# Kernel tuning notes

Measured on AMD Instinct MI355X. Metric: run time of the kernel, lower is better.

Reference implementation:

```python
import jax, jax.numpy as jnp
import numpy as np

B, N, D = 256, 128, 128            # batch, tree nodes (incl. zero-pad node 0), input_feature_dim
MAX_PRED, MAX_COL, MAX_OP = 30, 200, 20
OTHER = D - 2 * MAX_PRED - 1 - 32  # 35
C_IN = D + 64 - 2 * MAX_PRED - 1   # 131 = tree-conv input channels


def setup_inputs() -> dict:
    key = jax.random.key(0)
    ks = jax.random.split(key, 14)
    others = jax.random.normal(ks[0], (B, N, OTHER), dtype=jnp.float32)
    cols = jax.random.randint(ks[1], (B, N, MAX_PRED), 0, MAX_COL).astype(jnp.float32)
    ops = jax.random.randint(ks[2], (B, N, MAX_PRED), 0, MAX_OP).astype(jnp.float32)
    length = jax.random.randint(ks[3], (B, N, 1), 0, MAX_PRED + 1).astype(jnp.float32)
    param = jax.random.normal(ks[4], (B, N, 32), dtype=jnp.float32)
    feature = jnp.concatenate([others, cols, ops, length, param], axis=-1).transpose(0, 2, 1)  # (B, D, N)
    indexes = jax.random.randint(ks[5], (B, 3 * (N - 1), 1), 0, N, dtype=jnp.int32).astype(jnp.int64)

    def conv_w(k, o, i):
        return jax.random.normal(k, (o, i, 3), dtype=jnp.float32) * (1.0 / np.sqrt(3 * i))

    def lin_w(k, o, i):
        return jax.random.normal(k, (o, i), dtype=jnp.float32) * (1.0 / np.sqrt(i))

    return dict(
        feature=feature, indexes=indexes,
        col_embed=jax.random.normal(ks[6], (MAX_COL, 32), dtype=jnp.float32),
        op_embed=jax.random.normal(ks[7], (MAX_OP, 32), dtype=jnp.float32),
        w1=conv_w(ks[8], 256, C_IN), b1=jnp.zeros((256,), jnp.float32),
        w2=conv_w(ks[9], 128, 256), b2=jnp.zeros((128,), jnp.float32),
        w3=conv_w(ks[10], 64, 128), b3=jnp.zeros((64,), jnp.float32),
        fw1=lin_w(ks[11], 32, 64), fb1=jnp.zeros((32,), jnp.float32),
        fw2=lin_w(ks[12], 1, 32), fb2=jnp.zeros((1,), jnp.float32),
    )


def tree_conv(x, idx, w, b):
    # x: (B, C, N); idx: (B, 3M, 1) with M = N-1; w: (O, C, 3)
    Bb, C, _ = x.shape
    g = jnp.take_along_axis(x, idx[:, :, 0][:, None, :], axis=2)        # (B, C, 3M) gather (self,left,right)
    g = g.reshape(Bb, C, -1, 3)                                          # (B, C, M, 3)
    out = jnp.einsum('bcmk,ock->bom', g, w) + b[None, :, None]           # stride-3 kernel-3 conv
    zero = jnp.zeros((Bb, w.shape[0], 1), out.dtype)                     # re-prepend zero-pad node
    return jnp.concatenate([zero, out], axis=2)                          # (B, O, N)


def tree_norm(x):
    # per-sample layernorm over (channel, node) dims, unbiased std (torch.std default)
    mean = jnp.mean(x, axis=(1, 2), keepdims=True)
    std = jnp.std(x, axis=(1, 2), ddof=1, keepdims=True)
    return (x - mean) / (std + 1e-5)


def reference(feature, indexes, col_embed, op_embed, w1, b1, w2, b2, w3, b3, fw1, fb1, fw2, fb2):
    Bb, d, n = feature.shape
    f = feature.transpose(0, 2, 1).reshape(Bb * n, d)
    others = f[:, :OTHER]
    cols = jax.lax.stop_gradient(f[:, OTHER:OTHER + MAX_PRED]).astype(jnp.int32)
    ops = jax.lax.stop_gradient(f[:, OTHER + MAX_PRED:OTHER + 2 * MAX_PRED]).astype(jnp.int32)
    length = f[:, OTHER + 2 * MAX_PRED:OTHER + 2 * MAX_PRED + 1]          # (BN, 1)
    param = f[:, -32:]
    emb = jnp.concatenate([col_embed[cols], op_embed[ops]], axis=-1)      # (BN, P, 64)
    mask = jnp.arange(MAX_PRED)[None, :] < length                         # (BN, P)
    total = jnp.sum(emb * mask[..., None], axis=1)                        # (BN, 64) masked sum
    collate = jnp.concatenate([others, total, param], axis=-1).reshape(Bb, n, -1).transpose(0, 2, 1)  # (B, C_IN, N)

    x = jax.nn.leaky_relu(tree_norm(tree_conv(collate, indexes, w1, b1)), 0.01)
    x = jax.nn.leaky_relu(tree_norm(tree_conv(x, indexes, w2, b2)), 0.01)
    x = tree_norm(tree_conv(x, indexes, w3, b3))                          # (B, 64, N)
    pooled = jnp.max(x, axis=2)                                           # DynamicPooling -> (B, 64)
    h = jax.nn.relu(pooled @ fw1.T + fb1)
    return h @ fw2.T + fb2                                                # (B, 1)
```

## Files before the change

kernel.cpp:

```cpp
#include <hip/hip_runtime.h>
#include <hip/hip_bf16.h>
#include <math.h>

#define B_    256
#define N_    128
#define MAXP  30
#define OTHER_ 35
#define CIN1  131
#define NIDX  381

#define KPAD1 160
#define KPAD2 256
#define KPAD3 128
#define S_IDX (B_ * NIDX)
#define S_P1  (15 * 2 * 8 * 512)
#define S_P2  (24 * 2 * 4 * 512)
#define S_P3  (12 * 2 * 2 * 512)
#define PREP_TOTAL (S_IDX + S_P1 + S_P2 + S_P3)
#define PREP_BLOCKS ((PREP_TOTAL + 511) / 512)
#define EMBED_BLOCKS (B_ * 4)

typedef short short8 __attribute__((ext_vector_type(8)));
typedef float f32x4 __attribute__((ext_vector_type(4)));

__device__ inline void split1(float v, short& h, short& l) {
  unsigned u = __float_as_uint(v);
  unsigned hb = (u + 0x7fffu + ((u >> 16) & 1u)) >> 16;
  float fh = __uint_as_float(hb << 16);
  float r = v - fh;
  unsigned u2 = __float_as_uint(r);
  unsigned lb = (u2 + 0x7fffu + ((u2 >> 16) & 1u)) >> 16;
  h = (short)hb;
  l = (short)lb;
}

__device__ inline void split2(float v, short& h, short& l) {
  __hip_bfloat16 hb = __float2bfloat16(v);
  float fh = __bfloat162float(hb);
  __hip_bfloat16 lb = __float2bfloat16(v - fh);
  __builtin_memcpy(&h, &hb, 2);
  __builtin_memcpy(&l, &lb, 2);
}

template <int KREAL, int KPAD, int SUB, int NWO>
__device__ inline void packw(int l, const float* __restrict__ w,
                             short* __restrict__ oh, short* __restrict__ ol) {
  const int e = l & 7;
  const int lane = (l >> 3) & 63;
  const int x = l >> 9;
  const int su = x % SUB;
  const int y = x / SUB;
  const int g = y % NWO;
  const int gks = y / NWO;
  const int oc = (g * SUB + su) * 16 + (lane & 15);
  const int ctot = gks * 32 + ((lane >> 4) & 3) * 8 + e;
  const int kk = ctot / KPAD;
  const int ch = ctot - kk * KPAD;
  const float v = (ch < KREAL) ? w[(oc * KREAL + ch) * 3 + kk] : 0.f;
  short h, lo;
  split1(v, h, lo);
  oh[l] = h;
  ol[l] = lo;
}

__global__ __launch_bounds__(512) void prep_embed_kernel(
    const float* __restrict__ feature,
    const float* __restrict__ col_embed,
    const float* __restrict__ op_embed,
    short* __restrict__ collateH, short* __restrict__ collateL,
    const void* __restrict__ rawIdx, int* __restrict__ idx32,
    const float* __restrict__ w1, short* __restrict__ w1h, short* __restrict__ w1l,
    const float* __restrict__ w2, short* __restrict__ w2h, short* __restrict__ w2l,
    const float* __restrict__ w3, short* __restrict__ w3h, short* __restrict__ w3l) {
  const int bx = blockIdx.x;
  const int tid = threadIdx.x;

  if (bx >= EMBED_BLOCKS) {
    const int gid = (bx - EMBED_BLOCKS) * 512 + tid;
    if (gid < S_IDX) {
      const int* r32 = (const int*)rawIdx;
      const int lane = tid & 63;
      const int lo = r32[2 * lane];
      const int hi = r32[2 * lane + 1];
      const bool ok = (hi == 0 && lo >= 0 && lo < N_);
      const bool is64 = __all(ok);
      idx32[gid] = is64 ? (int)((const long long*)rawIdx)[gid] : ((const int*)rawIdx)[gid];
    } else if (gid < S_IDX + S_P1) {
      packw<131, KPAD1, 8, 2>(gid - S_IDX, w1, w1h, w1l);
    } else if (gid < S_IDX + S_P1 + S_P2) {
      packw<256, KPAD2, 4, 2>(gid - (S_IDX + S_P1), w2, w2h, w2l);
    } else if (gid < PREP_TOTAL) {
      packw<128, KPAD3, 2, 2>(gid - (S_IDX + S_P1 + S_P2), w3, w3h, w3l);
    }
    return;
  }

  __shared__ float feat[128 * 33];
  __shared__ float ce[200 * 32];
  __shared__ float oe[20 * 32];
  const int b = bx >> 2;
  const int n0 = (bx & 3) * 32;
  const float* fb = feature + (size_t)b * 16384;

  {
    const float4* s = (const float4*)col_embed;
    float4* d = (float4*)ce;
#pragma unroll
    for (int it = 0; it < 4; ++it) {
      const int t = it * 512 + tid;
      if (t < 1600) d[t] = s[t];
    }
    if (tid < 160) ((float4*)oe)[tid] = ((const float4*)op_embed)[tid];
  }
  {
    const int d = tid >> 2;
    const int c8 = (tid & 3) * 8;
    const float4 v0 = *reinterpret_cast<const float4*>(&fb[d * 128 + n0 + c8]);
    const float4 v1 = *reinterpret_cast<const float4*>(&fb[d * 128 + n0 + c8 + 4]);
    float* p = &feat[d * 33 + c8];
    p[0] = v0.x; p[1] = v0.y; p[2] = v0.z; p[3] = v0.w;
    p[4] = v1.x; p[5] = v1.y; p[6] = v1.z; p[7] = v1.w;
  }
  __syncthreads();

  const int wv = tid >> 6;
  const int lane = tid & 63;
  const int cl = lane & 31;

#pragma unroll
  for (int ni = 0; ni < 4; ++ni) {
    const int nl = wv * 4 + ni;
    const int n = n0 + nl;
    int civ = 0, oiv = 0;
    if (lane < MAXP) civ = (int)feat[(OTHER_ + lane) * 33 + nl];
    if (lane >= 32 && lane < 32 + MAXP) oiv = (int)feat[(OTHER_ + MAXP + (lane - 32)) * 33 + nl];
    const int L = (int)feat[95 * 33 + nl];

    float acc = 0.f;
    for (int i = 0; i < L; ++i) {
      const int cv = __shfl(civ, i);
      const int ov = __shfl(oiv, 32 + i);
      acc += (lane < 32) ? ce[cv * 32 + cl] : oe[ov * 32 + cl];
    }

    short* outH = collateH + ((size_t)b * 128 + n) * KPAD1;
    short* outL = collateL + ((size_t)b * 128 + n) * KPAD1;
    short h, l;
    split2(acc, h, l);
    outH[35 + lane] = h; outL[35 + lane] = l;
    if (lane < 35) {
      split2(feat[lane * 33 + nl], h, l);
      outH[lane] = h; outL[lane] = l;
    }
    if (lane < 32) {
      split2(feat[(96 + lane) * 33 + nl], h, l);
      outH[99 + lane] = h; outL[99 + lane] = l;
    }
    if (lane < 29) { outH[131 + lane] = 0; outL[131 + lane] = 0; }
  }
}

__global__ __launch_bounds__(512, 1) void fused_kernel(
    const short* __restrict__ XH, const short* __restrict__ XL,
    const int* __restrict__ idx,
    const short* __restrict__ w1h, const short* __restrict__ w1l,
    const short* __restrict__ w2h, const short* __restrict__ w2l,
    const short* __restrict__ w3h, const short* __restrict__ w3l,
    const float* __restrict__ b1, const float* __restrict__ b2,
    const float* __restrict__ b3,
    const float* __restrict__ fw1, const float* __restrict__ fb1,
    const float* __restrict__ fw2, const float* __restrict__ fb2,
    float* __restrict__ out) {
  constexpr int CINP = 72;

  __shared__ short sH[128 * CINP];
  __shared__ short sL[128 * CINP];
  __shared__ int nb_s[NIDX];
  __shared__ double red[16];
  __shared__ float bc[2];
  __shared__ float poolw[8][32];

  const int b = blockIdx.x;
  const int tid = threadIdx.x;
  const int lane = tid & 63;
  const int w = tid >> 6;
  const int wj = w >> 1;
  const int wo = w & 1;
  const int col = lane & 15;
  const int grp = (lane >> 4) & 3;
  const int jbase = wj * 32;

  const short8* __restrict__ wp1h = (const short8*)w1h;
  const short8* __restrict__ wp1l = (const short8*)w1l;
  const short8* __restrict__ wp2h = (const short8*)w2h;
  const short8* __restrict__ wp2l = (const short8*)w2l;
  const short8* __restrict__ wp3h = (const short8*)w3h;
  const short8* __restrict__ wp3l = (const short8*)w3l;

  const short* __restrict__ XHb = XH + (size_t)b * (128 * KPAD1);
  const short* __restrict__ XLb = XL + (size_t)b * (128 * KPAD1);
  short8 rh[2], rl[2];

  auto LOADS1 = [&](int s) {
    const int chb = s * 64;
    const int chn = (KPAD1 - chb < 64) ? (KPAD1 - chb) : 64;
    const int PKs = chn / 8;
#pragma unroll
    for (int it = 0; it < 2; ++it) {
      const int t = it * 512 + tid;
      if (t < 128 * PKs) {
        const int n = t / PKs;
        const int ch0 = chb + (t - n * PKs) * 8;
        rh[it] = *reinterpret_cast<const short8*>(&XHb[n * KPAD1 + ch0]);
        rl[it] = *reinterpret_cast<const short8*>(&XLb[n * KPAD1 + ch0]);
      }
    }
  };
  auto WRITES1 = [&](int s) {
    const int chb = s * 64;
    const int chn = (KPAD1 - chb < 64) ? (KPAD1 - chb) : 64;
    const int PKs = chn / 8;
#pragma unroll
    for (int it = 0; it < 2; ++it) {
      const int t = it * 512 + tid;
      if (t < 128 * PKs) {
        const int n = t / PKs;
        const int c0 = (t - n * PKs) * 8;
        *reinterpret_cast<short8*>(&sH[n * CINP + c0]) = rh[it];
        *reinterpret_cast<short8*>(&sL[n * CINP + c0]) = rl[it];
      }
    }
  };

  auto blockStats = [&](double ss, double sq, double cnt) {
#pragma unroll
    for (int o = 32; o > 0; o >>= 1) {
      ss += __shfl_down(ss, o, 64);
      sq += __shfl_down(sq, o, 64);
    }
    if (lane == 0) { red[w * 2] = ss; red[w * 2 + 1] = sq; }
    __syncthreads();
    if (tid == 0) {
      double S = 0.0, Q = 0.0;
#pragma unroll
      for (int i = 0; i < 8; ++i) { S += red[i * 2]; Q += red[i * 2 + 1]; }
      const double m = S / cnt;
      double var = (Q - S * S / cnt) / (cnt - 1.0);
      if (var < 0.0) var = 0.0;
      bc[0] = (float)m;
      bc[1] = (float)(1.0 / (sqrt(var) + 1e-5));
    }
    __syncthreads();
  };

  f32x4 a1[2][8];
#pragma unroll
  for (int jt = 0; jt < 2; ++jt)
#pragma unroll
    for (int su = 0; su < 8; ++su) {
      a1[jt][su][0] = 0.f; a1[jt][su][1] = 0.f;
      a1[jt][su][2] = 0.f; a1[jt][su][3] = 0.f;
    }

  LOADS1(0);
  if (tid < NIDX) nb_s[tid] = idx[b * NIDX + tid];
  WRITES1(0);
  __syncthreads();

  int nbr[2][3];
#pragma unroll
  for (int jt = 0; jt < 2; ++jt) {
    const int jA = jbase + jt * 16 + col;
#pragma unroll
    for (int kk = 0; kk < 3; ++kk)
      nbr[jt][kk] = (jA > 0) ? nb_s[(jA - 1) * 3 + kk] : 0;
  }

#pragma unroll
  for (int s = 0; s < 3; ++s) {
    if (s < 2) LOADS1(s + 1);
    const int nks = (s == 2) ? 1 : 2;
#pragma unroll
    for (int kk = 0; kk < 3; ++kk) {
      for (int q = 0; q < nks; ++q) {
        const int gks = kk * 5 + s * 2 + q;
        short8 ah[2], al[2];
#pragma unroll
        for (int jt = 0; jt < 2; ++jt) {
          const int ei = nbr[jt][kk] * CINP + q * 32 + grp * 8;
          ah[jt] = *reinterpret_cast<const short8*>(&sH[ei]);
          al[jt] = *reinterpret_cast<const short8*>(&sL[ei]);
        }
        short8 bh[8], bl[8];
#pragma unroll
        for (int su = 0; su < 8; ++su) {
          const int wi = ((gks * 2 + wo) * 8 + su) * 64 + lane;
          bh[su] = wp1h[wi];
          bl[su] = wp1l[wi];
        }
#pragma unroll
        for (int jt = 0; jt < 2; ++jt)
#pragma unroll
          for (int su = 0; su < 8; ++su) {
            a1[jt][su] = __builtin_amdgcn_mfma_f32_16x16x32_bf16(ah[jt], bh[su], a1[jt][su], 0, 0, 0);
            a1[jt][su] = __builtin_amdgcn_mfma_f32_16x16x32_bf16(al[jt], bh[su], a1[jt][su], 0, 0, 0);
            a1[jt][su] = __builtin_amdgcn_mfma_f32_16x16x32_bf16(ah[jt], bl[su], a1[jt][su], 0, 0, 0);
          }
      }
    }
    if (s < 2) {
      __syncthreads();
      WRITES1(s + 1);
      __syncthreads();
    }
  }

  {
    double ss = 0.0, sq = 0.0;
#pragma unroll
    for (int su = 0; su < 8; ++su) {
      const float bv = b1[(wo * 8 + su) * 16 + col];
#pragma unroll
      for (int jt = 0; jt < 2; ++jt)
#pragma unroll
        for (int r = 0; r < 4; ++r) {
          const int j = jbase + jt * 16 + grp * 4 + r;
          const float val = (j > 0) ? a1[jt][su][r] + bv : 0.f;
          a1[jt][su][r] = val;
          ss += (double)val;
          sq += (double)val * (double)val;
        }
    }
    blockStats(ss, sq, 256.0 * 128.0);
  }
  const float mean1 = bc[0], inv1 = bc[1];

  f32x4 a2[2][4];
#pragma unroll
  for (int jt = 0; jt < 2; ++jt)
#pragma unroll
    for (int su = 0; su < 4; ++su) {
      a2[jt][su][0] = 0.f; a2[jt][su][1] = 0.f;
      a2[jt][su][2] = 0.f; a2[jt][su][3] = 0.f;
    }

#pragma unroll
  for (int s = 0; s < 4; ++s) {
    __syncthreads();
    if (wo == (s >> 1)) {
#pragma unroll
      for (int u = 0; u < 4; ++u) {
        const int su1 = (s & 1) * 4 + u;
#pragma unroll
        for (int jt = 0; jt < 2; ++jt)
#pragma unroll
          for (int r = 0; r < 4; ++r) {
            const int j = jbase + jt * 16 + grp * 4 + r;
            float v = (a1[jt][su1][r] - mean1) * inv1;
            v = fmaxf(v, 0.01f * v);
            short h, l;
            split2(v, h, l);
            sH[j * CINP + u * 16 + col] = h;
            sL[j * CINP + u * 16 + col] = l;
          }
      }
    }
    __syncthreads();
#pragma unroll
    for (int kk = 0; kk < 3; ++kk)
#pragma unroll
      for (int q = 0; q < 2; ++q) {
        const int gks = kk * 8 + s * 2 + q;
        short8 ah[2], al[2];
#pragma unroll
        for (int jt = 0; jt < 2; ++jt) {
          const int ei = nbr[jt][kk] * CINP + q * 32 + grp * 8;
          ah[jt] = *reinterpret_cast<const short8*>(&sH[ei]);
          al[jt] = *reinterpret_cast<const short8*>(&sL[ei]);
        }
        short8 bh[4], bl[4];
#pragma unroll
        for (int su = 0; su < 4; ++su) {
          const int wi = ((gks * 2 + wo) * 4 + su) * 64 + lane;
          bh[su] = wp2h[wi];
          bl[su] = wp2l[wi];
        }
#pragma unroll
        for (int jt = 0; jt < 2; ++jt)
#pragma unroll
          for (int su = 0; su < 4; ++su) {
            a2[jt][su] = __builtin_amdgcn_mfma_f32_16x16x32_bf16(ah[jt], bh[su], a2[jt][su], 0, 0, 0);
            a2[jt][su] = __builtin_amdgcn_mfma_f32_16x16x32_bf16(al[jt], bh[su], a2[jt][su], 0, 0, 0);
            a2[jt][su] = __builtin_amdgcn_mfma_f32_16x16x32_bf16(ah[jt], bl[su], a2[jt][su], 0, 0, 0);
          }
      }
  }

  {
    double ss = 0.0, sq = 0.0;
#pragma unroll
    for (int su = 0; su < 4; ++su) {
      const float bv = b2[(wo * 4 + su) * 16 + col];
#pragma unroll
      for (int jt = 0; jt < 2; ++jt)
#pragma unroll
        for (int r = 0; r < 4; ++r) {
          const int j = jbase + jt * 16 + grp * 4 + r;
          const float val = (j > 0) ? a2[jt][su][r] + bv : 0.f;
          a2[jt][su][r] = val;
          ss += (double)val;
          sq += (double)val * (double)val;
        }
    }
    blockStats(ss, sq, 128.0 * 128.0);
  }
  const float mean2 = bc[0], inv2 = bc[1];

  f32x4 a3[2][2];
#pragma unroll
  for (int jt = 0; jt < 2; ++jt)
#pragma unroll
    for (int su = 0; su < 2; ++su) {
      a3[jt][su][0] = 0.f; a3[jt][su][1] = 0.f;
      a3[jt][su][2] = 0.f; a3[jt][su][3] = 0.f;
    }

#pragma unroll
  for (int s = 0; s < 2; ++s) {
    __syncthreads();
    if (wo == s) {
#pragma unroll
      for (int u = 0; u < 4; ++u) {
#pragma unroll
        for (int jt = 0; jt < 2; ++jt)
#pragma unroll
          for (int r = 0; r < 4; ++r) {
            const int j = jbase + jt * 16 + grp * 4 + r;
            float v = (a2[jt][u][r] - mean2) * inv2;
            v = fmaxf(v, 0.01f * v);
            short h, l;
            split2(v, h, l);
            sH[j * CINP + u * 16 + col] = h;
            sL[j * CINP + u * 16 + col] = l;
          }
      }
    }
    __syncthreads();
#pragma unroll
    for (int kk = 0; kk < 3; ++kk)
#pragma unroll
      for (int q = 0; q < 2; ++q) {
        const int gks = kk * 4 + s * 2 + q;
        short8 ah[2], al[2];
#pragma unroll
        for (int jt = 0; jt < 2; ++jt) {
          const int ei = nbr[jt][kk] * CINP + q * 32 + grp * 8;
          ah[jt] = *reinterpret_cast<const short8*>(&sH[ei]);
          al[jt] = *reinterpret_cast<const short8*>(&sL[ei]);
        }
        short8 bh[2], bl[2];
#pragma unroll
        for (int su = 0; su < 2; ++su) {
          const int wi = ((gks * 2 + wo) * 2 + su) * 64 + lane;
          bh[su] = wp3h[wi];
          bl[su] = wp3l[wi];
        }
#pragma unroll
        for (int jt = 0; jt < 2; ++jt)
#pragma unroll
          for (int su = 0; su < 2; ++su) {
            a3[jt][su] = __builtin_amdgcn_mfma_f32_16x16x32_bf16(ah[jt], bh[su], a3[jt][su], 0, 0, 0);
            a3[jt][su] = __builtin_amdgcn_mfma_f32_16x16x32_bf16(al[jt], bh[su], a3[jt][su], 0, 0, 0);
            a3[jt][su] = __builtin_amdgcn_mfma_f32_16x16x32_bf16(ah[jt], bl[su], a3[jt][su], 0, 0, 0);
          }
      }
  }

  {
    double ss = 0.0, sq = 0.0;
#pragma unroll
    for (int su = 0; su < 2; ++su) {
      const float bv = b3[(wo * 2 + su) * 16 + col];
#pragma unroll
      for (int jt = 0; jt < 2; ++jt)
#pragma unroll
        for (int r = 0; r < 4; ++r) {
          const int j = jbase + jt * 16 + grp * 4 + r;
          const float val = (j > 0) ? a3[jt][su][r] + bv : 0.f;
          a3[jt][su][r] = val;
          ss += (double)val;
          sq += (double)val * (double)val;
        }
    }
    blockStats(ss, sq, 64.0 * 128.0);
  }
  const float mean3 = bc[0], inv3 = bc[1];

#pragma unroll
  for (int su = 0; su < 2; ++su) {
    float pm = -3.4e38f;
#pragma unroll
    for (int jt = 0; jt < 2; ++jt)
#pragma unroll
      for (int r = 0; r < 4; ++r)
        pm = fmaxf(pm, (a3[jt][su][r] - mean3) * inv3);
    pm = fmaxf(pm, __shfl_xor(pm, 16, 64));
    pm = fmaxf(pm, __shfl_xor(pm, 32, 64));
    if (lane < 16) poolw[w][su * 16 + col] = pm;
  }
  __syncthreads();

  if (w == 0) {
    float hval = 0.f;
    if (lane < 32) {
      float a = fb1[lane];
#pragma unroll 8
      for (int c = 0; c < 64; ++c) {
        const int woc = c >> 5, loc = c & 31;
        float p = poolw[woc][loc];
#pragma unroll
        for (int jw = 1; jw < 4; ++jw) p = fmaxf(p, poolw[jw * 2 + woc][loc]);
        a = fmaf(p, fw1[lane * 64 + c], a);
      }
      hval = fmaxf(a, 0.f) * fw2[lane];
    }
#pragma unroll
    for (int o = 32; o > 0; o >>= 1) hval += __shfl_down(hval, o, 64);
    if (lane == 0) out[b] = hval + fb2[0];
  }
}

extern "C" void kernel_launch(void* const* d_in, const int* in_sizes, int n_in,
                              void* d_out, int out_size, void* d_ws, size_t ws_size,
                              hipStream_t stream) {
  const float* feature   = (const float*)d_in[0];
  const void*  indexes   = d_in[1];
  const float* col_embed = (const float*)d_in[2];
  const float* op_embed  = (const float*)d_in[3];
  const float* w1  = (const float*)d_in[4];
  const float* b1  = (const float*)d_in[5];
  const float* w2  = (const float*)d_in[6];
  const float* b2  = (const float*)d_in[7];
  const float* w3  = (const float*)d_in[8];
  const float* b3  = (const float*)d_in[9];
  const float* fw1 = (const float*)d_in[10];
  const float* fb1 = (const float*)d_in[11];
  const float* fw2 = (const float*)d_in[12];
  const float* fb2 = (const float*)d_in[13];
  float* out = (float*)d_out;

  char* ws = (char*)d_ws;
  size_t off = 0;
  auto carve = [&](size_t bytes) -> char* {
    off = (off + 255) & ~(size_t)255;
    char* p = ws + off;
    off += bytes;
    return p;
  };
  int*   idx32    = (int*)carve((size_t)S_IDX * sizeof(int));
  short* w1h      = (short*)carve((size_t)S_P1 * sizeof(short));
  short* w1l      = (short*)carve((size_t)S_P1 * sizeof(short));
  short* w2h      = (short*)carve((size_t)S_P2 * sizeof(short));
  short* w2l      = (short*)carve((size_t)S_P2 * sizeof(short));
  short* w3h      = (short*)carve((size_t)S_P3 * sizeof(short));
  short* w3l      = (short*)carve((size_t)S_P3 * sizeof(short));
  short* collateH = (short*)carve((size_t)B_ * 128 * KPAD1 * sizeof(short));
  short* collateL = (short*)carve((size_t)B_ * 128 * KPAD1 * sizeof(short));
  (void)ws_size; (void)in_sizes; (void)n_in; (void)out_size;

  hipLaunchKernelGGL(prep_embed_kernel, dim3(EMBED_BLOCKS + PREP_BLOCKS), dim3(512), 0, stream,
                     feature, col_embed, op_embed, collateH, collateL,
                     indexes, idx32, w1, w1h, w1l, w2, w2h, w2l, w3, w3h, w3l);
  hipLaunchKernelGGL(fused_kernel, dim3(B_), dim3(512), 0, stream,
                     collateH, collateL, idx32,
                     w1h, w1l, w2h, w2l, w3h, w3l,
                     b1, b2, b3, fw1, fb1, fw2, fb2, out);
}
```

Baseline: 86.06 us.

## Double fused kernel to 1024 threads and stage full activations in LDS

The fused tree-conv kernel now runs 16 waves per block instead of 8, splitting output channels four ways per wave group so each wave holds fewer accumulators. The LDS row stride grows to hold the full channel width, so each layer's input is written once and the chunked staging loops with their extra barriers go away. Weight packing is reshaped to match the new four-way output split. This costs much more LDS and enforces one block per CU, which may limit latency hiding.

```diff
diff --git a/kernel.cpp b/kernel.cpp
--- a/kernel.cpp
+++ b/kernel.cpp
@@ -13,9 +13,9 @@
 #define KPAD2 256
 #define KPAD3 128
 #define S_IDX (B_ * NIDX)
-#define S_P1  (15 * 2 * 8 * 512)
-#define S_P2  (24 * 2 * 4 * 512)
-#define S_P3  (12 * 2 * 2 * 512)
+#define S_P1  (15 * 4 * 4 * 512)
+#define S_P2  (24 * 4 * 2 * 512)
+#define S_P3  (12 * 4 * 1 * 512)
 #define PREP_TOTAL (S_IDX + S_P1 + S_P2 + S_P3)
 #define PREP_BLOCKS ((PREP_TOTAL + 511) / 512)
 #define EMBED_BLOCKS (B_ * 4)
@@ -86,11 +86,11 @@
       const bool is64 = __all(ok);
       idx32[gid] = is64 ? (int)((const long long*)rawIdx)[gid] : ((const int*)rawIdx)[gid];
     } else if (gid < S_IDX + S_P1) {
-      packw<131, KPAD1, 8, 2>(gid - S_IDX, w1, w1h, w1l);
+      packw<131, KPAD1, 4, 4>(gid - S_IDX, w1, w1h, w1l);
     } else if (gid < S_IDX + S_P1 + S_P2) {
-      packw<256, KPAD2, 4, 2>(gid - (S_IDX + S_P1), w2, w2h, w2l);
+      packw<256, KPAD2, 2, 4>(gid - (S_IDX + S_P1), w2, w2h, w2l);
     } else if (gid < PREP_TOTAL) {
-      packw<128, KPAD3, 2, 2>(gid - (S_IDX + S_P1 + S_P2), w3, w3h, w3l);
+      packw<128, KPAD3, 1, 4>(gid - (S_IDX + S_P1 + S_P2), w3, w3h, w3l);
     }
     return;
   }
@@ -160,7 +160,7 @@
   }
 }
 
-__global__ __launch_bounds__(512, 1) void fused_kernel(
+__global__ __launch_bounds__(1024, 1) void fused_kernel(
     const short* __restrict__ XH, const short* __restrict__ XL,
     const int* __restrict__ idx,
     const short* __restrict__ w1h, const short* __restrict__ w1l,
@@ -171,21 +171,21 @@
     const float* __restrict__ fw1, const float* __restrict__ fb1,
     const float* __restrict__ fw2, const float* __restrict__ fb2,
     float* __restrict__ out) {
-  constexpr int CINP = 72;
+  constexpr int CINP = 264;
 
   __shared__ short sH[128 * CINP];
   __shared__ short sL[128 * CINP];
   __shared__ int nb_s[NIDX];
-  __shared__ double red[16];
+  __shared__ double red[32];
   __shared__ float bc[2];
-  __shared__ float poolw[8][32];
+  __shared__ float poolw[16][16];
 
   const int b = blockIdx.x;
   const int tid = threadIdx.x;
   const int lane = tid & 63;
   const int w = tid >> 6;
-  const int wj = w >> 1;
-  const int wo = w & 1;
+  const int wj = w >> 2;
+  const int wo = w & 3;
   const int col = lane & 15;
   const int grp = (lane >> 4) & 3;
   const int jbase = wj * 32;
@@ -197,41 +197,6 @@
   const short8* __restrict__ wp3h = (const short8*)w3h;
   const short8* __restrict__ wp3l = (const short8*)w3l;
 
-  const short* __restrict__ XHb = XH + (size_t)b * (128 * KPAD1);
-  const short* __restrict__ XLb = XL + (size_t)b * (128 * KPAD1);
-  short8 rh[2], rl[2];
-
-  auto LOADS1 = [&](int s) {
-    const int chb = s * 64;
-    const int chn = (KPAD1 - chb < 64) ? (KPAD1 - chb) : 64;
-    const int PKs = chn / 8;
-#pragma unroll
-    for (int it = 0; it < 2; ++it) {
-      const int t = it * 512 + tid;
-      if (t < 128 * PKs) {
-        const int n = t / PKs;
-        const int ch0 = chb + (t - n * PKs) * 8;
-        rh[it] = *reinterpret_cast<const short8*>(&XHb[n * KPAD1 + ch0]);
-        rl[it] = *reinterpret_cast<const short8*>(&XLb[n * KPAD1 + ch0]);
-      }
-    }
-  };
-  auto WRITES1 = [&](int s) {
-    const int chb = s * 64;
-    const int chn = (KPAD1 - chb < 64) ? (KPAD1 - chb) : 64;
-    const int PKs = chn / 8;
-#pragma unroll
-    for (int it = 0; it < 2; ++it) {
-      const int t = it * 512 + tid;
-      if (t < 128 * PKs) {
-        const int n = t / PKs;
-        const int c0 = (t - n * PKs) * 8;
-        *reinterpret_cast<short8*>(&sH[n * CINP + c0]) = rh[it];
-        *reinterpret_cast<short8*>(&sL[n * CINP + c0]) = rl[it];
-      }
-    }
-  };
-
   auto blockStats = [&](double ss, double sq, double cnt) {
 #pragma unroll
     for (int o = 32; o > 0; o >>= 1) {
@@ -243,7 +208,7 @@
     if (tid == 0) {
       double S = 0.0, Q = 0.0;
 #pragma unroll
-      for (int i = 0; i < 8; ++i) { S += red[i * 2]; Q += red[i * 2 + 1]; }
+      for (int i = 0; i < 16; ++i) { S += red[i * 2]; Q += red[i * 2 + 1]; }
       const double m = S / cnt;
       double var = (Q - S * S / cnt) / (cnt - 1.0);
       if (var < 0.0) var = 0.0;
@@ -253,73 +218,78 @@
     __syncthreads();
   };
 
-  f32x4 a1[2][8];
+  {
+    const short* __restrict__ XHb = XH + (size_t)b * (128 * KPAD1);
+    const short* __restrict__ XLb = XL + (size_t)b * (128 * KPAD1);
+#pragma unroll
+    for (int it = 0; it < 3; ++it) {
+      const int t = it * 1024 + tid;
+      if (t < 128 * 20) {
+        const int n = t / 20;
+        const int c0 = (t - n * 20) * 8;
+        *reinterpret_cast<short8*>(&sH[n * CINP + c0]) =
+            *reinterpret_cast<const short8*>(&XHb[n * KPAD1 + c0]);
+        *reinterpret_cast<short8*>(&sL[n * CINP + c0]) =
+            *reinterpret_cast<const short8*>(&XLb[n * KPAD1 + c0]);
+      }
+    }
+  }
+  if (tid < NIDX) nb_s[tid] = idx[b * NIDX + tid];
+  __syncthreads();
+
+  int nbr[2][3];
+#pragma unroll
+  for (int jt = 0; jt < 2; ++jt) {
+    const int jA = jbase + jt * 16 + col;
+#pragma unroll
+    for (int kk = 0; kk < 3; ++kk)
+      nbr[jt][kk] = (jA > 0) ? nb_s[(jA - 1) * 3 + kk] : 0;
+  }
+
+  f32x4 a1[2][4];
 #pragma unroll
   for (int jt = 0; jt < 2; ++jt)
 #pragma unroll
-    for (int su = 0; su < 8; ++su) {
+    for (int su = 0; su < 4; ++su) {
       a1[jt][su][0] = 0.f; a1[jt][su][1] = 0.f;
       a1[jt][su][2] = 0.f; a1[jt][su][3] = 0.f;
     }
 
-  LOADS1(0);
-  if (tid < NIDX) nb_s[tid] = idx[b * NIDX + tid];
-  WRITES1(0);
-  __syncthreads();
-
-  int nbr[2][3];
-#pragma unroll
-  for (int jt = 0; jt < 2; ++jt) {
-    const int jA = jbase + jt * 16 + col;
-#pragma unroll
-    for (int kk = 0; kk < 3; ++kk)
-      nbr[jt][kk] = (jA > 0) ? nb_s[(jA - 1) * 3 + kk] : 0;
-  }
-
-#pragma unroll
-  for (int s = 0; s < 3; ++s) {
-    if (s < 2) LOADS1(s + 1);
-    const int nks = (s == 2) ? 1 : 2;
-#pragma unroll
-    for (int kk = 0; kk < 3; ++kk) {
-      for (int q = 0; q < nks; ++q) {
-        const int gks = kk * 5 + s * 2 + q;
-        short8 ah[2], al[2];
-#pragma unroll
-        for (int jt = 0; jt < 2; ++jt) {
-          const int ei = nbr[jt][kk] * CINP + q * 32 + grp * 8;
-          ah[jt] = *reinterpret_cast<const short8*>(&sH[ei]);
-          al[jt] = *reinterpret_cast<const short8*>(&sL[ei]);
+#pragma unroll
+  for (int kk = 0; kk < 3; ++kk) {
+#pragma unroll
+    for (int ks = 0; ks < 5; ++ks) {
+      const int gks = kk * 5 + ks;
+      short8 ah[2], al[2];
+#pragma unroll
+      for (int jt = 0; jt < 2; ++jt) {
+        const int ei = nbr[jt][kk] * CINP + ks * 32 + grp * 8;
+        ah[jt] = *reinterpret_cast<const short8*>(&sH[ei]);
+        al[jt] = *reinterpret_cast<const short8*>(&sL[ei]);
+      }
+      short8 bh[4], bl[4];
+#pragma unroll
+      for (int su = 0; su < 4; ++su) {
+        const int wi = ((gks * 4 + wo) * 4 + su) * 64 + lane;
+        bh[su] = wp1h[wi];
+        bl[su] = wp1l[wi];
+      }
+#pragma unroll
+      for (int jt = 0; jt < 2; ++jt)
+#pragma unroll
+        for (int su = 0; su < 4; ++su) {
+          a1[jt][su] = __builtin_amdgcn_mfma_f32_16x16x32_bf16(ah[jt], bh[su], a1[jt][su], 0, 0, 0);
+          a1[jt][su] = __builtin_amdgcn_mfma_f32_16x16x32_bf16(al[jt], bh[su], a1[jt][su], 0, 0, 0);
+          a1[jt][su] = __builtin_amdgcn_mfma_f32_16x16x32_bf16(ah[jt], bl[su], a1[jt][su], 0, 0, 0);
         }
-        short8 bh[8], bl[8];
-#pragma unroll
-        for (int su = 0; su < 8; ++su) {
-          const int wi = ((gks * 2 + wo) * 8 + su) * 64 + lane;
-          bh[su] = wp1h[wi];
-          bl[su] = wp1l[wi];
-        }
-#pragma unroll
-        for (int jt = 0; jt < 2; ++jt)
-#pragma unroll
-          for (int su = 0; su < 8; ++su) {
-            a1[jt][su] = __builtin_amdgcn_mfma_f32_16x16x32_bf16(ah[jt], bh[su], a1[jt][su], 0, 0, 0);
-            a1[jt][su] = __builtin_amdgcn_mfma_f32_16x16x32_bf16(al[jt], bh[su], a1[jt][su], 0, 0, 0);
-            a1[jt][su] = __builtin_amdgcn_mfma_f32_16x16x32_bf16(ah[jt], bl[su], a1[jt][su], 0, 0, 0);
-          }
-      }
-    }
-    if (s < 2) {
-      __syncthreads();
-      WRITES1(s + 1);
-      __syncthreads();
     }
   }
 
   {
     double ss = 0.0, sq = 0.0;
 #pragma unroll
-    for (int su = 0; su < 8; ++su) {
-      const float bv = b1[(wo * 8 + su) * 16 + col];
+    for (int su = 0; su < 4; ++su) {
+      const float bv = b1[(wo * 4 + su) * 16 + col];
 #pragma unroll
       for (int jt = 0; jt < 2; ++jt)
 #pragma unroll
@@ -335,72 +305,68 @@
   }
   const float mean1 = bc[0], inv1 = bc[1];
 
-  f32x4 a2[2][4];
+#pragma unroll
+  for (int su = 0; su < 4; ++su) {
+    const int c = (wo * 4 + su) * 16 + col;
+#pragma unroll
+    for (int jt = 0; jt < 2; ++jt)
+#pragma unroll
+      for (int r = 0; r < 4; ++r) {
+        const int j = jbase + jt * 16 + grp * 4 + r;
+        float v = (a1[jt][su][r] - mean1) * inv1;
+        v = fmaxf(v, 0.01f * v);
+        short h, l;
+        split2(v, h, l);
+        sH[j * CINP + c] = h;
+        sL[j * CINP + c] = l;
+      }
+  }
+  __syncthreads();
+
+  f32x4 a2[2][2];
 #pragma unroll
   for (int jt = 0; jt < 2; ++jt)
 #pragma unroll
-    for (int su = 0; su < 4; ++su) {
+    for (int su = 0; su < 2; ++su) {
       a2[jt][su][0] = 0.f; a2[jt][su][1] = 0.f;
       a2[jt][su][2] = 0.f; a2[jt][su][3] = 0.f;
     }
 
 #pragma unroll
-  for (int s = 0; s < 4; ++s) {
-    __syncthreads();
-    if (wo == (s >> 1)) {
-#pragma unroll
-      for (int u = 0; u < 4; ++u) {
-        const int su1 = (s & 1) * 4 + u;
-#pragma unroll
-        for (int jt = 0; jt < 2; ++jt)
-#pragma unroll
-          for (int r = 0; r < 4; ++r) {
-            const int j = jbase + jt * 16 + grp * 4 + r;
-            float v = (a1[jt][su1][r] - mean1) * inv1;
-            v = fmaxf(v, 0.01f * v);
-            short h, l;
-            split2(v, h, l);
-            sH[j * CINP + u * 16 + col] = h;
-            sL[j * CINP + u * 16 + col] = l;
-          }
-      }
-    }
-    __syncthreads();
-#pragma unroll
-    for (int kk = 0; kk < 3; ++kk)
-#pragma unroll
-      for (int q = 0; q < 2; ++q) {
-        const int gks = kk * 8 + s * 2 + q;
-        short8 ah[2], al[2];
-#pragma unroll
-        for (int jt = 0; jt < 2; ++jt) {
-          const int ei = nbr[jt][kk] * CINP + q * 32 + grp * 8;
-          ah[jt] = *reinterpret_cast<const short8*>(&sH[ei]);
-          al[jt] = *reinterpret_cast<const short8*>(&sL[ei]);
+  for (int kk = 0; kk < 3; ++kk) {
+#pragma unroll
+    for (int ks = 0; ks < 8; ++ks) {
+      const int gks = kk * 8 + ks;
+      short8 ah[2], al[2];
+#pragma unroll
+      for (int jt = 0; jt < 2; ++jt) {
+        const int ei = nbr[jt][kk] * CINP + ks * 32 + grp * 8;
+        ah[jt] = *reinterpret_cast<const short8*>(&sH[ei]);
+        al[jt] = *reinterpret_cast<const short8*>(&sL[ei]);
+      }
+      short8 bh[2], bl[2];
+#pragma unroll
+      for (int su = 0; su < 2; ++su) {
+        const int wi = ((gks * 4 + wo) * 2 + su) * 64 + lane;
+        bh[su] = wp2h[wi];
+        bl[su] = wp2l[wi];
+      }
+#pragma unroll
+      for (int jt = 0; jt < 2; ++jt)
+#pragma unroll
+        for (int su = 0; su < 2; ++su) {
+          a2[jt][su] = __builtin_amdgcn_mfma_f32_16x16x32_bf16(ah[jt], bh[su], a2[jt][su], 0, 0, 0);
+          a2[jt][su] = __builtin_amdgcn_mfma_f32_16x16x32_bf16(al[jt], bh[su], a2[jt][su], 0, 0, 0);
+          a2[jt][su] = __builtin_amdgcn_mfma_f32_16x16x32_bf16(ah[jt], bl[su], a2[jt][su], 0, 0, 0);
         }
-        short8 bh[4], bl[4];
-#pragma unroll
-        for (int su = 0; su < 4; ++su) {
-          const int wi = ((gks * 2 + wo) * 4 + su) * 64 + lane;
-          bh[su] = wp2h[wi];
-          bl[su] = wp2l[wi];
-        }
-#pragma unroll
-        for (int jt = 0; jt < 2; ++jt)
-#pragma unroll
-          for (int su = 0; su < 4; ++su) {
-            a2[jt][su] = __builtin_amdgcn_mfma_f32_16x16x32_bf16(ah[jt], bh[su], a2[jt][su], 0, 0, 0);
-            a2[jt][su] = __builtin_amdgcn_mfma_f32_16x16x32_bf16(al[jt], bh[su], a2[jt][su], 0, 0, 0);
-            a2[jt][su] = __builtin_amdgcn_mfma_f32_16x16x32_bf16(ah[jt], bl[su], a2[jt][su], 0, 0, 0);
-          }
-      }
+    }
   }
 
   {
     double ss = 0.0, sq = 0.0;
 #pragma unroll
-    for (int su = 0; su < 4; ++su) {
-      const float bv = b2[(wo * 4 + su) * 16 + col];
+    for (int su = 0; su < 2; ++su) {
+      const float bv = b2[(wo * 2 + su) * 16 + col];
 #pragma unroll
       for (int jt = 0; jt < 2; ++jt)
 #pragma unroll
@@ -416,97 +382,84 @@
   }
   const float mean2 = bc[0], inv2 = bc[1];
 
-  f32x4 a3[2][2];
-#pragma unroll
-  for (int jt = 0; jt < 2; ++jt)
-#pragma unroll
-    for (int su = 0; su < 2; ++su) {
-      a3[jt][su][0] = 0.f; a3[jt][su][1] = 0.f;
-      a3[jt][su][2] = 0.f; a3[jt][su][3] = 0.f;
-    }
-
-#pragma unroll
-  for (int s = 0; s < 2; ++s) {
-    __syncthreads();
-    if (wo == s) {
-#pragma unroll
-      for (int u = 0; u < 4; ++u) {
-#pragma unroll
-        for (int jt = 0; jt < 2; ++jt)
-#pragma unroll
-          for (int r = 0; r < 4; ++r) {
-            const int j = jbase + jt * 16 + grp * 4 + r;
-            float v = (a2[jt][u][r] - mean2) * inv2;
-            v = fmaxf(v, 0.01f * v);
-            short h, l;
-            split2(v, h, l);
-            sH[j * CINP + u * 16 + col] = h;
-            sL[j * CINP + u * 16 + col] = l;
-          }
-      }
-    }
-    __syncthreads();
-#pragma unroll
-    for (int kk = 0; kk < 3; ++kk)
-#pragma unroll
-      for (int q = 0; q < 2; ++q) {
-        const int gks = kk * 4 + s * 2 + q;
-        short8 ah[2], al[2];
-#pragma unroll
-        for (int jt = 0; jt < 2; ++jt) {
-          const int ei = nbr[jt][kk] * CINP + q * 32 + grp * 8;
-          ah[jt] = *reinterpret_cast<const short8*>(&sH[ei]);
-          al[jt] = *reinterpret_cast<const short8*>(&sL[ei]);
-        }
-        short8 bh[2], bl[2];
-#pragma unroll
-        for (int su = 0; su < 2; ++su) {
-          const int wi = ((gks * 2 + wo) * 2 + su) * 64 + lane;
-          bh[su] = wp3h[wi];
-          bl[su] = wp3l[wi];
-        }
-#pragma unroll
-        for (int jt = 0; jt < 2; ++jt)
-#pragma unroll
-          for (int su = 0; su < 2; ++su) {
-            a3[jt][su] = __builtin_amdgcn_mfma_f32_16x16x32_bf16(ah[jt], bh[su], a3[jt][su], 0, 0, 0);
-            a3[jt][su] = __builtin_amdgcn_mfma_f32_16x16x32_bf16(al[jt], bh[su], a3[jt][su], 0, 0, 0);
-            a3[jt][su] = __builtin_amdgcn_mfma_f32_16x16x32_bf16(ah[jt], bl[su], a3[jt][su], 0, 0, 0);
-          }
-      }
+#pragma unroll
+  for (int su = 0; su < 2; ++su) {
+    const int c = (wo * 2 + su) * 16 + col;
+#pragma unroll
+    for (int jt = 0; jt < 2; ++jt)
+#pragma unroll
+      for (int r = 0; r < 4; ++r) {
+        const int j = jbase + jt * 16 + grp * 4 + r;
+        float v = (a2[jt][su][r] - mean2) * inv2;
+        v = fmaxf(v, 0.01f * v);
+        short h, l;
+        split2(v, h, l);
+        sH[j * CINP + c] = h;
+        sL[j * CINP + c] = l;
+      }
+  }
+  __syncthreads();
+
+  f32x4 a3[2];
+#pragma unroll
+  for (int jt = 0; jt < 2; ++jt) {
+    a3[jt][0] = 0.f; a3[jt][1] = 0.f; a3[jt][2] = 0.f; a3[jt][3] = 0.f;
+  }
+
+#pragma unroll
+  for (int kk = 0; kk < 3; ++kk) {
+#pragma unroll
+    for (int ks = 0; ks < 4; ++ks) {
+      const int gks = kk * 4 + ks;
+      short8 ah[2], al[2];
+#pragma unroll
+      for (int jt = 0; jt < 2; ++jt) {
+        const int ei = nbr[jt][kk] * CINP + ks * 32 + grp * 8;
+        ah[jt] = *reinterpret_cast<const short8*>(&sH[ei]);
+        al[jt] = *reinterpret_cast<const short8*>(&sL[ei]);
+      }
+      short8 bh, bl;
+      {
+        const int wi = (gks * 4 + wo) * 64 + lane;
+        bh = wp3h[wi];
+        bl = wp3l[wi];
+      }
+#pragma unroll
+      for (int jt = 0; jt < 2; ++jt) {
+        a3[jt] = __builtin_amdgcn_mfma_f32_16x16x32_bf16(ah[jt], bh, a3[jt], 0, 0, 0);
+        a3[jt] = __builtin_amdgcn_mfma_f32_16x16x32_bf16(al[jt], bh, a3[jt], 0, 0, 0);
+        a3[jt] = __builtin_amdgcn_mfma_f32_16x16x32_bf16(ah[jt], bl, a3[jt], 0, 0, 0);
+      }
+    }
   }
 
   {
     double ss = 0.0, sq = 0.0;
-#pragma unroll
-    for (int su = 0; su < 2; ++su) {
-      const float bv = b3[(wo * 2 + su) * 16 + col];
-#pragma unroll
-      for (int jt = 0; jt < 2; ++jt)
-#pragma unroll
-        for (int r = 0; r < 4; ++r) {
-          const int j = jbase + jt * 16 + grp * 4 + r;
-          const float val = (j > 0) ? a3[jt][su][r] + bv : 0.f;
-          a3[jt][su][r] = val;
-          ss += (double)val;
-          sq += (double)val * (double)val;
-        }
-    }
+    const float bv = b3[wo * 16 + col];
+#pragma unroll
+    for (int jt = 0; jt < 2; ++jt)
+#pragma unroll
+      for (int r = 0; r < 4; ++r) {
+        const int j = jbase + jt * 16 + grp * 4 + r;
+        const float val = (j > 0) ? a3[jt][r] + bv : 0.f;
+        a3[jt][r] = val;
+        ss += (double)val;
+        sq += (double)val * (double)val;
+      }
     blockStats(ss, sq, 64.0 * 128.0);
   }
   const float mean3 = bc[0], inv3 = bc[1];
 
-#pragma unroll
-  for (int su = 0; su < 2; ++su) {
+  {
     float pm = -3.4e38f;
 #pragma unroll
     for (int jt = 0; jt < 2; ++jt)
 #pragma unroll
       for (int r = 0; r < 4; ++r)
-        pm = fmaxf(pm, (a3[jt][su][r] - mean3) * inv3);
+        pm = fmaxf(pm, (a3[jt][r] - mean3) * inv3);
     pm = fmaxf(pm, __shfl_xor(pm, 16, 64));
     pm = fmaxf(pm, __shfl_xor(pm, 32, 64));
-    if (lane < 16) poolw[w][su * 16 + col] = pm;
+    if (lane < 16) poolw[w][col] = pm;
   }
   __syncthreads();
 
@@ -516,10 +469,10 @@
       float a = fb1[lane];
 #pragma unroll 8
       for (int c = 0; c < 64; ++c) {
-        const int woc = c >> 5, loc = c & 31;
-        float p = poolw[woc][loc];
-#pragma unroll
-        for (int jw = 1; jw < 4; ++jw) p = fmaxf(p, poolw[jw * 2 + woc][loc]);
+        const int oq = c >> 4, oc16 = c & 15;
+        float p = poolw[oq][oc16];
+#pragma unroll
+        for (int jw = 1; jw < 4; ++jw) p = fmaxf(p, poolw[jw * 4 + oq][oc16]);
         a = fmaf(p, fw1[lane * 64 + c], a);
       }
       hval = fmaxf(a, 0.f) * fw2[lane];
@@ -571,7 +524,7 @@
   hipLaunchKernelGGL(prep_embed_kernel, dim3(EMBED_BLOCKS + PREP_BLOCKS), dim3(512), 0, stream,
                      feature, col_embed, op_embed, collateH, collateL,
                      indexes, idx32, w1, w1h, w1l, w2, w2h, w2l, w3, w3h, w3l);
-  hipLaunchKernelGGL(fused_kernel, dim3(B_), dim3(512), 0, stream,
+  hipLaunchKernelGGL(fused_kernel, dim3(B_), dim3(1024), 0, stream,
                      collateH, collateL, idx32,
                      w1h, w1l, w2h, w2l, w3h, w3l,
                      b1, b2, b3, fw1, fb1, fw2, fb2, out);
```

Result: faster. 84.23 us (-2.1%).
